# Kernel optimization log

Hardware: AMD Instinct MI355X
Metric: run time of the kernel (lower is better)

Reference implementation:

```python
import jax, jax.numpy as jnp
import numpy as np

H = 160      # hidden_size
NH = 8       # num_heads
HD = H // NH # per_head_size = 20
MAXLEN = 512 # max_seq_len (pe tables have 2*MAXLEN+1 rows)
FF = 640     # ffn inner size
B, S = 4, 256


def setup_inputs():
    key = jax.random.key(0)
    ks = jax.random.split(key, 24)
    def rn(k, shape, scale=0.02):
        return jax.random.normal(k, shape, dtype=jnp.float32) * scale
    tbl = 2 * MAXLEN + 1
    d = dict(
        inp=jax.random.normal(ks[0], (B, S, H), dtype=jnp.float32),
        pos_s=jnp.sort(jax.random.randint(ks[1], (B, S), 0, S), axis=-1),
        pos_e=jnp.sort(jax.random.randint(ks[2], (B, S), 0, S), axis=-1),
        seq_len=jax.random.randint(ks[3], (B,), S // 2, S + 1),
        lex_num=0,
        pe_ss=rn(ks[4], (tbl, H), 1.0), pe_se=rn(ks[5], (tbl, H), 1.0),
        pe_es=rn(ks[6], (tbl, H), 1.0), pe_ee=rn(ks[7], (tbl, H), 1.0),
        W_fus=rn(ks[8], (4 * H, H)), b_fus=jnp.zeros((H,), jnp.float32),
        Wq=rn(ks[9], (H, H)), bq=jnp.zeros((H,), jnp.float32),
        Wk=rn(ks[10], (H, H)), bk=jnp.zeros((H,), jnp.float32),
        Wv=rn(ks[11], (H, H)), bv=jnp.zeros((H,), jnp.float32),
        Wr=rn(ks[12], (H, H)), br=jnp.zeros((H,), jnp.float32),
        u=rn(ks[13], (NH, HD), 0.1), v=rn(ks[14], (NH, HD), 0.1),
        W_fin=rn(ks[15], (H, H)), b_fin=jnp.zeros((H,), jnp.float32),
        ln1_g=jnp.ones((H,), jnp.float32), ln1_b=jnp.zeros((H,), jnp.float32),
        W1=rn(ks[16], (H, FF)), b1=jnp.zeros((FF,), jnp.float32),
        W2=rn(ks[17], (FF, H)), b2=jnp.zeros((H,), jnp.float32),
        ln2_g=jnp.ones((H,), jnp.float32), ln2_b=jnp.zeros((H,), jnp.float32),
    )
    return d


def _ln(x, g, b, eps=1e-5):
    mu = jnp.mean(x, axis=-1, keepdims=True)
    var = jnp.mean((x - mu) ** 2, axis=-1, keepdims=True)
    return (x - mu) * jax.lax.rsqrt(var + eps) * g + b


def reference(inp, pos_s, pos_e, seq_len, lex_num, pe_ss, pe_se, pe_es, pe_ee,
              W_fus, b_fus, Wq, bq, Wk, bk, Wv, bv, Wr, br, u, v,
              W_fin, b_fin, ln1_g, ln1_b, W1, b1, W2, b2, ln2_g, ln2_b):
    Bb, Ss, Hh = inp.shape
    # ---- Four_Pos_Fusion_Embedding, fusion='ff' ----
    dss = pos_s[:, :, None] - pos_s[:, None, :] + MAXLEN  # [B,S,S] indices
    dse = pos_s[:, :, None] - pos_e[:, None, :] + MAXLEN
    des = pos_e[:, :, None] - pos_s[:, None, :] + MAXLEN
    dee = pos_e[:, :, None] - pos_e[:, None, :] + MAXLEN
    pe4 = jnp.concatenate([pe_ss[dss], pe_se[dse], pe_es[des], pe_ee[dee]], axis=-1)  # [B,S,S,4H]
    rel = jax.nn.relu(pe4 @ W_fus + b_fus)  # [B,S,S,H]
    # ---- MultiHead_Attention_Lattice_rel (Transformer-XL style) ----
    q = (inp @ Wq + bq).reshape(Bb, Ss, NH, HD).transpose(0, 2, 1, 3)   # [B,H,S,d]
    k = (inp @ Wk + bk).reshape(Bb, Ss, NH, HD).transpose(0, 2, 1, 3)
    val = (inp @ Wv + bv).reshape(Bb, Ss, NH, HD).transpose(0, 2, 1, 3)
    r = (rel @ Wr + br).reshape(Bb, Ss, Ss, NH, HD)                     # [B,Sq,Sk,H,d]
    A_C = jnp.einsum('bhid,bhjd->bhij', q + u[None, :, None, :], k)
    B_D = jnp.einsum('bhid,bijhd->bhij', q + v[None, :, None, :], r)
    scores = (A_C + B_D) / np.float32(np.sqrt(HD))
    mask = jnp.arange(Ss)[None, :] < (seq_len + lex_num)[:, None]       # [B,S]
    scores = jnp.where(mask[:, None, None, :], scores, jnp.float32(-1e15))
    attn = jax.nn.softmax(scores, axis=-1)
    out = jnp.einsum('bhij,bhjd->bhid', attn, val)
    out = out.transpose(0, 2, 1, 3).reshape(Bb, Ss, Hh)
    out = out @ W_fin + b_fin
    # ---- Layer_Process 'an': output = LN(output + output) (as written in source) ----
    out = _ln(out + out, ln1_g, ln1_b)
    # ---- PositionWise_FeedForward ----
    ff = jax.nn.relu(out @ W1 + b1) @ W2 + b2
    out2 = _ln(ff + ff, ln2_g, ln2_b)
    return out2
```

## Files before the change

### kernel.cpp

```cpp
#include <hip/hip_runtime.h>
#include <hip/hip_bf16.h>
#include <math.h>

#define SS    256
#define BB    4
#define HH    160
#define NH_   8
#define HD_   20
#define TBL   1025
#define MAXL  512
#define FF_   640
#define PROWS 512

#define PT_TILES 64
#define PT_PER_TAB (PT_TILES * 3)
#define PT_END (4 * PT_PER_TAB)
#define QKV_END (PT_END + 512)
#define WRT_END (QKV_END + 100)

__device__ __forceinline__ float blo(unsigned x) {
  return __uint_as_float(x << 16);
}
__device__ __forceinline__ float bhi(unsigned x) {
  return __uint_as_float(x & 0xffff0000u);
}

__global__ __launch_bounds__(256) void k_setup(
    const float* __restrict__ pe_ss, const float* __restrict__ pe_se,
    const float* __restrict__ pe_es, const float* __restrict__ pe_ee,
    const float* __restrict__ W_fus, const float* __restrict__ b_fus,
    const float* __restrict__ inp,
    const float* __restrict__ Wq, const float* __restrict__ bq,
    const float* __restrict__ Wk, const float* __restrict__ bk,
    const float* __restrict__ Wv, const float* __restrict__ bv,
    const float* __restrict__ Wr,
    __hip_bfloat16* __restrict__ Pbf, float* __restrict__ qb,
    float* __restrict__ kb, float* __restrict__ vb, float* __restrict__ WrT) {
  int bid = blockIdx.x;
  int t = threadIdx.x;
  __shared__ __align__(16) float As[16][HH];

  if (bid < PT_END) {
    int tab = bid / PT_PER_TAB;
    int rem = bid - tab * PT_PER_TAB;
    int tile = rem / 3, yc = rem - tile * 3;
    int row0 = 256 + tile * 8;
    const float* pe = (tab == 0) ? pe_ss : (tab == 1) ? pe_se
                    : (tab == 2) ? pe_es : pe_ee;
    for (int idx = t; idx < 8 * 40; idx += 256) {
      int r = idx / 40, c4 = idx - r * 40;
      *(float4*)&As[r][c4 * 4] =
          *(const float4*)(pe + (size_t)(row0 + r) * HH + c4 * 4);
    }
    __syncthreads();
    int c = (t & 63) + yc * 64;
    int wv = t >> 6;
    if (c < HH) {
      float acc0, acc1;
      acc0 = acc1 = (tab == 0) ? b_fus[c] : 0.0f;
      const float* wp = W_fus + (size_t)tab * HH * HH + c;
      int r0 = wv * 2, r1 = wv * 2 + 1;
      #pragma unroll 2
      for (int k = 0; k < HH; k += 8) {
        float w[8];
        #pragma unroll
        for (int q = 0; q < 8; ++q) w[q] = wp[(size_t)(k + q) * HH];
        float4 a0 = *(const float4*)&As[r0][k];
        float4 a1 = *(const float4*)&As[r0][k + 4];
        float4 b0 = *(const float4*)&As[r1][k];
        float4 b1_ = *(const float4*)&As[r1][k + 4];
        acc0 = fmaf(a0.x, w[0], acc0); acc0 = fmaf(a0.y, w[1], acc0);
        acc0 = fmaf(a0.z, w[2], acc0); acc0 = fmaf(a0.w, w[3], acc0);
        acc0 = fmaf(a1.x, w[4], acc0); acc0 = fmaf(a1.y, w[5], acc0);
        acc0 = fmaf(a1.z, w[6], acc0); acc0 = fmaf(a1.w, w[7], acc0);
        acc1 = fmaf(b0.x, w[0], acc1); acc1 = fmaf(b0.y, w[1], acc1);
        acc1 = fmaf(b0.z, w[2], acc1); acc1 = fmaf(b0.w, w[3], acc1);
        acc1 = fmaf(b1_.x, w[4], acc1); acc1 = fmaf(b1_.y, w[5], acc1);
        acc1 = fmaf(b1_.z, w[6], acc1); acc1 = fmaf(b1_.w, w[7], acc1);
      }
      int rloc = tile * 8;
      Pbf[((size_t)tab * PROWS + rloc + r0) * HH + c] = __float2bfloat16(acc0);
      Pbf[((size_t)tab * PROWS + rloc + r1) * HH + c] = __float2bfloat16(acc1);
    }
  } else if (bid < QKV_END) {
    int qbid = bid - PT_END;
    int bx = qbid & 63, by = qbid >> 6;
    int tok0 = bx * 16;
    {
      const float4* src = (const float4*)(inp + (size_t)tok0 * HH);
      float4* dst = (float4*)As;
      for (int idx = t; idx < 16 * HH / 4; idx += 256) dst[idx] = src[idx];
    }
    __syncthreads();
    int col = (t & 63) + by * 64;
    int wv = t >> 6;
    if (col < 480) {
      int mat = col / 160;
      int c = col - mat * 160;
      const float* W   = (mat == 0) ? Wq : (mat == 1) ? Wk : Wv;
      const float* bia = (mat == 0) ? bq : (mat == 1) ? bk : bv;
      float* O         = (mat == 0) ? qb : (mat == 1) ? kb : vb;
      float acc[4];
      float bb = bia[c];
      #pragma unroll
      for (int i = 0; i < 4; ++i) acc[i] = bb;
      const float* wp = W + c;
      #pragma unroll 2
      for (int k = 0; k < HH; k += 8) {
        float w[8];
        #pragma unroll
        for (int q = 0; q < 8; ++q) w[q] = wp[(size_t)(k + q) * HH];
        #pragma unroll
        for (int i = 0; i < 4; ++i) {
          const float4 a0 = *(const float4*)&As[wv * 4 + i][k];
          const float4 a1 = *(const float4*)&As[wv * 4 + i][k + 4];
          acc[i] = fmaf(a0.x, w[0], acc[i]);
          acc[i] = fmaf(a0.y, w[1], acc[i]);
          acc[i] = fmaf(a0.z, w[2], acc[i]);
          acc[i] = fmaf(a0.w, w[3], acc[i]);
          acc[i] = fmaf(a1.x, w[4], acc[i]);
          acc[i] = fmaf(a1.y, w[5], acc[i]);
          acc[i] = fmaf(a1.z, w[6], acc[i]);
          acc[i] = fmaf(a1.w, w[7], acc[i]);
        }
      }
      #pragma unroll
      for (int i = 0; i < 4; ++i)
        O[(size_t)(tok0 + wv * 4 + i) * HH + c] = acc[i];
    }
  } else {
    int o = (bid - QKV_END) * 256 + t;
    int cp = o / HH, cc = o - cp * HH;
    WrT[o] = Wr[(size_t)cc * HH + cp];
  }
}

__global__ __launch_bounds__(256) void k_gmat(
    const float* __restrict__ qb, const float* __restrict__ vtab,
    const float* __restrict__ WrT, __hip_bfloat16* __restrict__ gmat_bf) {
  const int T = 4;
  int tok0 = blockIdx.x * T;
  int t = threadIdx.x;
  __shared__ __align__(16) float qs[T][HH];
  if (t < T * HH / 4) {
    int tt = t / 40, c4 = t - tt * 40;
    float4 q4 = *(const float4*)(qb + (size_t)(tok0 + tt) * HH + c4 * 4);
    float4 v4 = *(const float4*)(vtab + c4 * 4);
    q4.x += v4.x; q4.y += v4.y; q4.z += v4.z; q4.w += v4.w;
    *(float4*)&qs[tt][c4 * 4] = q4;
  }
  __syncthreads();
  #pragma unroll
  for (int r = 0; r < 5; ++r) {
    int p = r * 256 + t;
    int h = p / HH, cc = p - h * HH;
    float acc0 = 0.f, acc1 = 0.f, acc2 = 0.f, acc3 = 0.f;
    const float* wp = WrT + (size_t)(h * HD_) * HH + cc;
    #pragma unroll 4
    for (int d = 0; d < HD_; ++d) {
      float w = wp[(size_t)d * HH];
      acc0 = fmaf(qs[0][h * HD_ + d], w, acc0);
      acc1 = fmaf(qs[1][h * HD_ + d], w, acc1);
      acc2 = fmaf(qs[2][h * HD_ + d], w, acc2);
      acc3 = fmaf(qs[3][h * HD_ + d], w, acc3);
    }
    gmat_bf[(size_t)(tok0 + 0) * (NH_ * HH) + p] = __float2bfloat16(acc0);
    gmat_bf[(size_t)(tok0 + 1) * (NH_ * HH) + p] = __float2bfloat16(acc1);
    gmat_bf[(size_t)(tok0 + 2) * (NH_ * HH) + p] = __float2bfloat16(acc2);
    gmat_bf[(size_t)(tok0 + 3) * (NH_ * HH) + p] = __float2bfloat16(acc3);
  }
}

template<int TT, int KK, bool RELU>
__global__ __launch_bounds__(256) void k_gemm(
    const float* __restrict__ A, const float* __restrict__ W,
    const float* __restrict__ bias, float* __restrict__ C, int N) {
  const int TPW = TT / 4;
  int tok0 = blockIdx.x * TT;
  int t = threadIdx.x;
  __shared__ __align__(16) float As[TT][KK];
  {
    const float4* src = (const float4*)(A + (size_t)tok0 * KK);
    float4* dst = (float4*)As;
    for (int idx = t; idx < TT * KK / 4; idx += 256) dst[idx] = src[idx];
  }
  __syncthreads();
  int c = (t & 63) + blockIdx.y * 64;
  int wv = t >> 6;
  if (c < N) {
    float acc[TPW];
    float bb = bias ? bias[c] : 0.0f;
    #pragma unroll
    for (int i = 0; i < TPW; ++i) acc[i] = bb;
    const float* wp = W + c;
    #pragma unroll 2
    for (int k = 0; k < KK; k += 8) {
      float w[8];
      #pragma unroll
      for (int q = 0; q < 8; ++q) w[q] = wp[(size_t)(k + q) * N];
      #pragma unroll
      for (int i = 0; i < TPW; ++i) {
        const float4 a0 = *(const float4*)&As[wv * TPW + i][k];
        const float4 a1 = *(const float4*)&As[wv * TPW + i][k + 4];
        acc[i] = fmaf(a0.x, w[0], acc[i]);
        acc[i] = fmaf(a0.y, w[1], acc[i]);
        acc[i] = fmaf(a0.z, w[2], acc[i]);
        acc[i] = fmaf(a0.w, w[3], acc[i]);
        acc[i] = fmaf(a1.x, w[4], acc[i]);
        acc[i] = fmaf(a1.y, w[5], acc[i]);
        acc[i] = fmaf(a1.z, w[6], acc[i]);
        acc[i] = fmaf(a1.w, w[7], acc[i]);
      }
    }
    #pragma unroll
    for (int i = 0; i < TPW; ++i) {
      float v = RELU ? fmaxf(acc[i], 0.0f) : acc[i];
      C[(size_t)(tok0 + wv * TPW + i) * N + c] = v;
    }
  }
}

__global__ __launch_bounds__(256) void k_ffn1(
    const float* __restrict__ Y, const float* __restrict__ g1,
    const float* __restrict__ b1ln, const float* __restrict__ W1,
    const float* __restrict__ b1, float* __restrict__ Hb) {
  const int TT = 16;
  int tok0 = blockIdx.x * TT;
  int t = threadIdx.x;
  __shared__ __align__(16) float As[TT][HH];
  {
    const float4* src = (const float4*)(Y + (size_t)tok0 * HH);
    float4* dst = (float4*)As;
    for (int idx = t; idx < TT * HH / 4; idx += 256) dst[idx] = src[idx];
  }
  __syncthreads();
  {
    int row = t >> 4, l = t & 15;
    float s = 0.0f;
    #pragma unroll
    for (int c = l; c < HH; c += 16) s += As[row][c];
    #pragma unroll
    for (int m = 1; m < 16; m <<= 1) s += __shfl_xor(s, m);
    float mu = s * (1.0f / HH);
    float s2 = 0.0f;
    #pragma unroll
    for (int c = l; c < HH; c += 16) { float d = As[row][c] - mu; s2 = fmaf(d, d, s2); }
    #pragma unroll
    for (int m = 1; m < 16; m <<= 1) s2 += __shfl_xor(s2, m);
    float rstd = rsqrtf(s2 * (1.0f / HH) + 2.5e-6f);
    #pragma unroll
    for (int c = l; c < HH; c += 16)
      As[row][c] = (As[row][c] - mu) * rstd * g1[c] + b1ln[c];
  }
  __syncthreads();
  int c = (t & 63) + blockIdx.y * 64;
  int wv = t >> 6;
  float acc[4];
  float bb = b1[c];
  #pragma unroll
  for (int i = 0; i < 4; ++i) acc[i] = bb;
  const float* wp = W1 + c;
  #pragma unroll 2
  for (int k = 0; k < HH; k += 8) {
    float w[8];
    #pragma unroll
    for (int q = 0; q < 8; ++q) w[q] = wp[(size_t)(k + q) * FF_];
    #pragma unroll
    for (int i = 0; i < 4; ++i) {
      const float4 a0 = *(const float4*)&As[wv * 4 + i][k];
      const float4 a1 = *(const float4*)&As[wv * 4 + i][k + 4];
      acc[i] = fmaf(a0.x, w[0], acc[i]);
      acc[i] = fmaf(a0.y, w[1], acc[i]);
      acc[i] = fmaf(a0.z, w[2], acc[i]);
      acc[i] = fmaf(a0.w, w[3], acc[i]);
      acc[i] = fmaf(a1.x, w[4], acc[i]);
      acc[i] = fmaf(a1.y, w[5], acc[i]);
      acc[i] = fmaf(a1.z, w[6], acc[i]);
      acc[i] = fmaf(a1.w, w[7], acc[i]);
    }
  }
  #pragma unroll
  for (int i = 0; i < 4; ++i)
    Hb[(size_t)(tok0 + wv * 4 + i) * FF_ + c] = fmaxf(acc[i], 0.0f);
}

#define RSTR 164
#define SCP  132

__global__ __launch_bounds__(256, 4) void k_score(
    const float* __restrict__ qb, const float* __restrict__ kb,
    const __hip_bfloat16* __restrict__ gmat_bf,
    const __hip_bfloat16* __restrict__ Pbf,
    const int* __restrict__ pos_s, const int* __restrict__ pos_e,
    const int* __restrict__ seq_len, const int* __restrict__ lex_num,
    const float* __restrict__ utab, float* __restrict__ scores) {
  int bid = blockIdx.x;
  int blk = bid >> 1;
  int half = bid & 1;
  int b = blk >> 8;
  int i = blk & 255;
  int t = threadIdx.x;
  int limit = seq_len[b] + lex_num[0];
  if (half * 128 >= limit) return;

  __shared__ __align__(16) float qu[HH];
  __shared__ __align__(16) float g_s[NH_][RSTR];
  __shared__ __align__(16) float sc_s[NH_][SCP];
  __shared__ int ps_s[SS], pe_s[SS];

  if (t < HH) qu[t] = qb[(size_t)blk * HH + t] + utab[t];
  ps_s[t] = pos_s[b * SS + t];
  pe_s[t] = pos_e[b * SS + t];
  if (t < 160) {
    const uint4* gsrc = (const uint4*)(gmat_bf + (size_t)blk * (NH_ * HH));
    uint4 u = gsrc[t];
    int h = t / 20, c8 = (t - h * 20) * 8;
    g_s[h][c8 + 0] = blo(u.x); g_s[h][c8 + 1] = bhi(u.x);
    g_s[h][c8 + 2] = blo(u.y); g_s[h][c8 + 3] = bhi(u.y);
    g_s[h][c8 + 4] = blo(u.z); g_s[h][c8 + 5] = bhi(u.z);
    g_s[h][c8 + 6] = blo(u.w); g_s[h][c8 + 7] = bhi(u.w);
  }
  __syncthreads();

  int w = t >> 6, lane = t & 63;
  int jj = lane >> 2, cg = lane & 3;
  int psi = ps_s[i], pei = pe_s[i];
  const float scale = 0.22360679774997896f;

  const uint4* Pb0 = (const uint4*)Pbf;
  const uint4* Pb1 = Pb0 + (size_t)PROWS * 20;
  const uint4* Pb2 = Pb1 + (size_t)PROWS * 20;
  const uint4* Pb3 = Pb2 + (size_t)PROWS * 20;
  const float4* kb4 = (const float4*)(kb + (size_t)b * SS * HH);

  #pragma unroll
  for (int pass = 0; pass < 2; ++pass) {
    int tau = (pass == 0) ? w : 7 - w;
    int jl = tau * 16 + jj;
    int j = half * 128 + jl;
    if (half * 128 + tau * 16 >= limit) continue;
    int psj = ps_s[j], pej = pe_s[j];
    int r0b = (psi - psj + 256) * 20;
    int r1b = (psi - pej + 256) * 20;
    int r2b = (pei - psj + 256) * 20;
    int r3b = (pei - pej + 256) * 20;
    float bd[NH_];
    #pragma unroll
    for (int h = 0; h < NH_; ++h) bd[h] = 0.0f;
    #pragma unroll 2
    for (int q5 = 0; q5 < 5; ++q5) {
      int off = q5 * 4 + cg;
      uint4 u0 = Pb0[r0b + off];
      uint4 u1 = Pb1[r1b + off];
      uint4 u2 = Pb2[r2b + off];
      uint4 u3 = Pb3[r3b + off];
      float rl[8];
      rl[0] = fmaxf(blo(u0.x) + blo(u1.x) + blo(u2.x) + blo(u3.x), 0.0f);
      rl[1] = fmaxf(bhi(u0.x) + bhi(u1.x) + bhi(u2.x) + bhi(u3.x), 0.0f);
      rl[2] = fmaxf(blo(u0.y) + blo(u1.y) + blo(u2.y) + blo(u3.y), 0.0f);
      rl[3] = fmaxf(bhi(u0.y) + bhi(u1.y) + bhi(u2.y) + bhi(u3.y), 0.0f);
      rl[4] = fmaxf(blo(u0.z) + blo(u1.z) + blo(u2.z) + blo(u3.z), 0.0f);
      rl[5] = fmaxf(bhi(u0.z) + bhi(u1.z) + bhi(u2.z) + bhi(u3.z), 0.0f);
      rl[6] = fmaxf(blo(u0.w) + blo(u1.w) + blo(u2.w) + blo(u3.w), 0.0f);
      rl[7] = fmaxf(bhi(u0.w) + bhi(u1.w) + bhi(u2.w) + bhi(u3.w), 0.0f);
      int cb = off * 8;
      #pragma unroll
      for (int h = 0; h < NH_; ++h) {
        float4 ga = *(const float4*)&g_s[h][cb];
        float4 gb = *(const float4*)&g_s[h][cb + 4];
        bd[h] = fmaf(rl[0], ga.x, bd[h]);
        bd[h] = fmaf(rl[1], ga.y, bd[h]);
        bd[h] = fmaf(rl[2], ga.z, bd[h]);
        bd[h] = fmaf(rl[3], ga.w, bd[h]);
        bd[h] = fmaf(rl[4], gb.x, bd[h]);
        bd[h] = fmaf(rl[5], gb.y, bd[h]);
        bd[h] = fmaf(rl[6], gb.z, bd[h]);
        bd[h] = fmaf(rl[7], gb.w, bd[h]);
      }
    }
    float ac0 = 0.0f, ac1 = 0.0f;
    {
      int kbase = j * 40 + 10 * cg;
      #pragma unroll
      for (int m = 0; m < 10; ++m) {
        float4 kv = kb4[kbase + m];
        float4 q4 = *(const float4*)&qu[(10 * cg + m) * 4];
        if (m < 5) {
          ac0 = fmaf(q4.x, kv.x, ac0); ac0 = fmaf(q4.y, kv.y, ac0);
          ac0 = fmaf(q4.z, kv.z, ac0); ac0 = fmaf(q4.w, kv.w, ac0);
        } else {
          ac1 = fmaf(q4.x, kv.x, ac1); ac1 = fmaf(q4.y, kv.y, ac1);
          ac1 = fmaf(q4.z, kv.z, ac1); ac1 = fmaf(q4.w, kv.w, ac1);
        }
      }
    }
    #pragma unroll
    for (int h = 0; h < NH_; ++h) {
      bd[h] += __shfl_xor(bd[h], 1);
      bd[h] += __shfl_xor(bd[h], 2);
    }
    float s0, s1;
    if      (cg == 0) { s0 = bd[0]; s1 = bd[1]; }
    else if (cg == 1) { s0 = bd[2]; s1 = bd[3]; }
    else if (cg == 2) { s0 = bd[4]; s1 = bd[5]; }
    else              { s0 = bd[6]; s1 = bd[7]; }
    sc_s[2 * cg][jl]     = (s0 + ac0) * scale;
    sc_s[2 * cg + 1][jl] = (s1 + ac1) * scale;
  }
  __syncthreads();

  {
    int row = t >> 5, c4 = t & 31;
    float4 v = *(const float4*)&sc_s[row][c4 * 4];
    *(float4*)&scores[((size_t)blk * NH_ + row) * SS + half * 128 + c4 * 4] = v;
  }
}

#define SCS 260

__global__ __launch_bounds__(256, 4) void k_smpv(
    const float* __restrict__ scores, const float* __restrict__ vb,
    const int* __restrict__ seq_len, const int* __restrict__ lex_num,
    const float* __restrict__ W_fin, const float* __restrict__ b_fin,
    float* __restrict__ ybuf) {
  int blk = blockIdx.x;
  int b = blk >> 8;
  int t = threadIdx.x;
  __shared__ __align__(16) float sc[NH_][SCS];
  __shared__ __align__(16) float outs[HH];
  int limit = seq_len[b] + lex_num[0];

  const float4* src = (const float4*)(scores + (size_t)blk * NH_ * SS);
  #pragma unroll
  for (int r = 0; r < 2; ++r) {
    int idx = r * 256 + t;
    int row = idx >> 6, c4 = idx & 63;
    float4 v = src[idx];
    int j0 = c4 * 4;
    v.x = (j0 + 0 < limit) ? v.x : -1.0e15f;
    v.y = (j0 + 1 < limit) ? v.y : -1.0e15f;
    v.z = (j0 + 2 < limit) ? v.z : -1.0e15f;
    v.w = (j0 + 3 < limit) ? v.w : -1.0e15f;
    *(float4*)&sc[row][j0] = v;
  }
  __syncthreads();

  {
    int h = t >> 5, l = t & 31;
    float m = -3.0e38f;
    float e[8];
    #pragma unroll
    for (int ii = 0; ii < 8; ++ii) m = fmaxf(m, sc[h][l + ii * 32]);
    #pragma unroll
    for (int msk = 16; msk; msk >>= 1) m = fmaxf(m, __shfl_xor(m, msk));
    float s = 0.0f;
    #pragma unroll
    for (int ii = 0; ii < 8; ++ii) { e[ii] = __expf(sc[h][l + ii * 32] - m); s += e[ii]; }
    #pragma unroll
    for (int msk = 16; msk; msk >>= 1) s += __shfl_xor(s, msk);
    float inv = 1.0f / s;
    #pragma unroll
    for (int ii = 0; ii < 8; ++ii) sc[h][l + ii * 32] = e[ii] * inv;
  }
  __syncthreads();

  if (t < HH) {
    int h = t / HD_;
    int lim4 = (limit + 3) & ~3;
    float acc0 = 0.f, acc1 = 0.f, acc2 = 0.f, acc3 = 0.f;
    const float* vcol = vb + (size_t)b * SS * HH + t;
    for (int j2 = 0; j2 < lim4; j2 += 4) {
      float4 p4 = *(const float4*)&sc[h][j2];
      acc0 = fmaf(p4.x, vcol[(size_t)(j2 + 0) * HH], acc0);
      acc1 = fmaf(p4.y, vcol[(size_t)(j2 + 1) * HH], acc1);
      acc2 = fmaf(p4.z, vcol[(size_t)(j2 + 2) * HH], acc2);
      acc3 = fmaf(p4.w, vcol[(size_t)(j2 + 3) * HH], acc3);
    }
    outs[t] = (acc0 + acc1) + (acc2 + acc3);
  }
  __syncthreads();

  if (t < HH) {
    float acc = b_fin[t];
    const float* wp = W_fin + t;
    #pragma unroll 8
    for (int c = 0; c < HH; ++c)
      acc = fmaf(outs[c], wp[(size_t)c * HH], acc);
    ybuf[(size_t)blk * HH + t] = acc;
  }
}

__global__ __launch_bounds__(256) void k_ln(
    const float* __restrict__ Y, const float* __restrict__ g,
    const float* __restrict__ bln, float* __restrict__ O) {
  int tok = blockIdx.x * 4 + (threadIdx.x >> 6);
  int l = threadIdx.x & 63;
  const float* y = Y + (size_t)tok * HH;
  float a = y[l];
  float bv = y[l + 64];
  bool has3 = l < (HH - 128);
  float cv = has3 ? y[l + 128] : 0.0f;
  float s = a + bv + cv;
  #pragma unroll
  for (int m = 32; m; m >>= 1) s += __shfl_xor(s, m);
  float mu = s * (1.0f / HH);
  float da = a - mu, db = bv - mu, dc = has3 ? (cv - mu) : 0.0f;
  float s2 = da * da + db * db + dc * dc;
  #pragma unroll
  for (int m = 32; m; m >>= 1) s2 += __shfl_xor(s2, m);
  float rstd = rsqrtf(s2 * (1.0f / HH) + 2.5e-6f);
  float* o = O + (size_t)tok * HH;
  o[l]      = da * rstd * g[l] + bln[l];
  o[l + 64] = db * rstd * g[l + 64] + bln[l + 64];
  if (has3) o[l + 128] = dc * rstd * g[l + 128] + bln[l + 128];
}

extern "C" void kernel_launch(void* const* d_in, const int* in_sizes, int n_in,
                              void* d_out, int out_size, void* d_ws, size_t ws_size,
                              hipStream_t stream) {
  const float* inp    = (const float*)d_in[0];
  const int*   pos_s  = (const int*)d_in[1];
  const int*   pos_e  = (const int*)d_in[2];
  const int*   seq_ln = (const int*)d_in[3];
  const int*   lex_nm = (const int*)d_in[4];
  const float* pe_ss  = (const float*)d_in[5];
  const float* pe_se  = (const float*)d_in[6];
  const float* pe_es  = (const float*)d_in[7];
  const float* pe_ee  = (const float*)d_in[8];
  const float* W_fus  = (const float*)d_in[9];
  const float* b_fus  = (const float*)d_in[10];
  const float* Wq     = (const float*)d_in[11];
  const float* bq     = (const float*)d_in[12];
  const float* Wk     = (const float*)d_in[13];
  const float* bk     = (const float*)d_in[14];
  const float* Wv     = (const float*)d_in[15];
  const float* bv     = (const float*)d_in[16];
  const float* Wr     = (const float*)d_in[17];
  const float* utab   = (const float*)d_in[19];
  const float* vtab   = (const float*)d_in[20];
  const float* W_fin  = (const float*)d_in[21];
  const float* b_fin  = (const float*)d_in[22];
  const float* ln1_g  = (const float*)d_in[23];
  const float* ln1_b  = (const float*)d_in[24];
  const float* W1     = (const float*)d_in[25];
  const float* b1     = (const float*)d_in[26];
  const float* W2     = (const float*)d_in[27];
  const float* b2     = (const float*)d_in[28];
  const float* ln2_g  = (const float*)d_in[29];
  const float* ln2_b  = (const float*)d_in[30];

  float* ws = (float*)d_ws;
  __hip_bfloat16* Pbf = (__hip_bfloat16*)ws;
  float* qb       = ws + 163840;
  float* kb       = qb + BB * SS * HH;
  float* vb       = kb + BB * SS * HH;
  float* WrT      = vb + BB * SS * HH;
  float* gregion  = WrT + HH * HH;
  __hip_bfloat16* gmat_bf = (__hip_bfloat16*)gregion;
  float* ybuf     = gregion;
  float* scores   = gregion + 655360;
  float* hbuf     = scores;
  float* y2       = scores + 655360;

  (void)in_sizes; (void)n_in; (void)out_size; (void)ws_size;

  const int M = BB * SS;

  k_setup<<<WRT_END, 256, 0, stream>>>(pe_ss, pe_se, pe_es, pe_ee, W_fus, b_fus,
                                       inp, Wq, bq, Wk, bk, Wv, bv, Wr,
                                       Pbf, qb, kb, vb, WrT);
  k_gmat<<<M / 4, 256, 0, stream>>>(qb, vtab, WrT, gmat_bf);
  k_score<<<2 * M, 256, 0, stream>>>(qb, kb, gmat_bf, Pbf, pos_s, pos_e,
                                     seq_ln, lex_nm, utab, scores);
  k_smpv<<<M, 256, 0, stream>>>(scores, vb, seq_ln, lex_nm, W_fin, b_fin, ybuf);
  k_ffn1<<<dim3(M / 16, 10), 256, 0, stream>>>(ybuf, ln1_g, ln1_b, W1, b1, hbuf);
  k_gemm<4, FF_, false><<<dim3(M / 4, 3), 256, 0, stream>>>(hbuf, W2, b2, y2, HH);
  k_ln<<<M / 4, 256, 0, stream>>>(y2, ln2_g, ln2_b, (float*)d_out);
}
```

Baseline: 114.8 us.

## Split score kernel into quarter-row blocks and split-K the W2 GEMM

Result: no change. 115.3 us (+0.4%).

```diff
diff --git a/kernel.cpp b/kernel.cpp
--- a/kernel.cpp
+++ b/kernel.cpp
@@ -171,55 +171,6 @@
   }
 }
 
-template<int TT, int KK, bool RELU>
-__global__ __launch_bounds__(256) void k_gemm(
-    const float* __restrict__ A, const float* __restrict__ W,
-    const float* __restrict__ bias, float* __restrict__ C, int N) {
-  const int TPW = TT / 4;
-  int tok0 = blockIdx.x * TT;
-  int t = threadIdx.x;
-  __shared__ __align__(16) float As[TT][KK];
-  {
-    const float4* src = (const float4*)(A + (size_t)tok0 * KK);
-    float4* dst = (float4*)As;
-    for (int idx = t; idx < TT * KK / 4; idx += 256) dst[idx] = src[idx];
-  }
-  __syncthreads();
-  int c = (t & 63) + blockIdx.y * 64;
-  int wv = t >> 6;
-  if (c < N) {
-    float acc[TPW];
-    float bb = bias ? bias[c] : 0.0f;
-    #pragma unroll
-    for (int i = 0; i < TPW; ++i) acc[i] = bb;
-    const float* wp = W + c;
-    #pragma unroll 2
-    for (int k = 0; k < KK; k += 8) {
-      float w[8];
-      #pragma unroll
-      for (int q = 0; q < 8; ++q) w[q] = wp[(size_t)(k + q) * N];
-      #pragma unroll
-      for (int i = 0; i < TPW; ++i) {
-        const float4 a0 = *(const float4*)&As[wv * TPW + i][k];
-        const float4 a1 = *(const float4*)&As[wv * TPW + i][k + 4];
-        acc[i] = fmaf(a0.x, w[0], acc[i]);
-        acc[i] = fmaf(a0.y, w[1], acc[i]);
-        acc[i] = fmaf(a0.z, w[2], acc[i]);
-        acc[i] = fmaf(a0.w, w[3], acc[i]);
-        acc[i] = fmaf(a1.x, w[4], acc[i]);
-        acc[i] = fmaf(a1.y, w[5], acc[i]);
-        acc[i] = fmaf(a1.z, w[6], acc[i]);
-        acc[i] = fmaf(a1.w, w[7], acc[i]);
-      }
-    }
-    #pragma unroll
-    for (int i = 0; i < TPW; ++i) {
-      float v = RELU ? fmaxf(acc[i], 0.0f) : acc[i];
-      C[(size_t)(tok0 + wv * TPW + i) * N + c] = v;
-    }
-  }
-}
-
 __global__ __launch_bounds__(256) void k_ffn1(
     const float* __restrict__ Y, const float* __restrict__ g1,
     const float* __restrict__ b1ln, const float* __restrict__ W1,
@@ -284,8 +235,51 @@
     Hb[(size_t)(tok0 + wv * 4 + i) * FF_ + c] = fmaxf(acc[i], 0.0f);
 }
 
+__global__ __launch_bounds__(256) void k_w2(
+    const float* __restrict__ A, const float* __restrict__ W2,
+    const float* __restrict__ b2, float* __restrict__ y2a,
+    float* __restrict__ y2b) {
+  const int TT = 4, KH = 320;
+  int tok0 = blockIdx.x * TT;
+  int kz = blockIdx.z;
+  int t = threadIdx.x;
+  __shared__ __align__(16) float As[TT][KH];
+  {
+    const float* src = A + (size_t)tok0 * FF_ + kz * KH;
+    for (int idx = t; idx < TT * KH / 4; idx += 256) {
+      int tt = idx / (KH / 4), c4 = idx - tt * (KH / 4);
+      *(float4*)&As[tt][c4 * 4] = *(const float4*)(src + (size_t)tt * FF_ + c4 * 4);
+    }
+  }
+  __syncthreads();
+  int c = (t & 63) + blockIdx.y * 64;
+  int wv = t >> 6;
+  if (c < HH) {
+    float acc = (kz == 0) ? b2[c] : 0.0f;
+    const float* wp = W2 + (size_t)(kz * KH) * HH + c;
+    #pragma unroll 2
+    for (int k = 0; k < KH; k += 8) {
+      float w[8];
+      #pragma unroll
+      for (int q = 0; q < 8; ++q) w[q] = wp[(size_t)(k + q) * HH];
+      const float4 a0 = *(const float4*)&As[wv][k];
+      const float4 a1 = *(const float4*)&As[wv][k + 4];
+      acc = fmaf(a0.x, w[0], acc);
+      acc = fmaf(a0.y, w[1], acc);
+      acc = fmaf(a0.z, w[2], acc);
+      acc = fmaf(a0.w, w[3], acc);
+      acc = fmaf(a1.x, w[4], acc);
+      acc = fmaf(a1.y, w[5], acc);
+      acc = fmaf(a1.z, w[6], acc);
+      acc = fmaf(a1.w, w[7], acc);
+    }
+    float* O = (kz == 0) ? y2a : y2b;
+    O[(size_t)(tok0 + wv) * HH + c] = acc;
+  }
+}
+
 #define RSTR 164
-#define SCP  132
+#define SCP  68
 
 __global__ __launch_bounds__(256, 4) void k_score(
     const float* __restrict__ qb, const float* __restrict__ kb,
@@ -295,13 +289,13 @@
     const int* __restrict__ seq_len, const int* __restrict__ lex_num,
     const float* __restrict__ utab, float* __restrict__ scores) {
   int bid = blockIdx.x;
-  int blk = bid >> 1;
-  int half = bid & 1;
+  int blk = bid >> 2;
+  int qtr = bid & 3;
   int b = blk >> 8;
   int i = blk & 255;
   int t = threadIdx.x;
   int limit = seq_len[b] + lex_num[0];
-  if (half * 128 >= limit) return;
+  if (qtr * 64 >= limit) return;
 
   __shared__ __align__(16) float qu[HH];
   __shared__ __align__(16) float g_s[NH_][RSTR];
@@ -333,12 +327,9 @@
   const uint4* Pb3 = Pb2 + (size_t)PROWS * 20;
   const float4* kb4 = (const float4*)(kb + (size_t)b * SS * HH);
 
-  #pragma unroll
-  for (int pass = 0; pass < 2; ++pass) {
-    int tau = (pass == 0) ? w : 7 - w;
-    int jl = tau * 16 + jj;
-    int j = half * 128 + jl;
-    if (half * 128 + tau * 16 >= limit) continue;
+  int jl = w * 16 + jj;
+  int j = qtr * 64 + jl;
+  if (qtr * 64 + w * 16 < limit) {
     int psj = ps_s[j], pej = pe_s[j];
     int r0b = (psi - psj + 256) * 20;
     int r1b = (psi - pej + 256) * 20;
@@ -409,10 +400,10 @@
   }
   __syncthreads();
 
-  {
-    int row = t >> 5, c4 = t & 31;
+  if (t < 128) {
+    int row = t >> 4, c4 = t & 15;
     float4 v = *(const float4*)&sc_s[row][c4 * 4];
-    *(float4*)&scores[((size_t)blk * NH_ + row) * SS + half * 128 + c4 * 4] = v;
+    *(float4*)&scores[((size_t)blk * NH_ + row) * SS + qtr * 64 + c4 * 4] = v;
   }
 }
 
@@ -490,16 +481,18 @@
   }
 }
 
-__global__ __launch_bounds__(256) void k_ln(
-    const float* __restrict__ Y, const float* __restrict__ g,
-    const float* __restrict__ bln, float* __restrict__ O) {
+__global__ __launch_bounds__(256) void k_ln2(
+    const float* __restrict__ Ya, const float* __restrict__ Yb,
+    const float* __restrict__ g, const float* __restrict__ bln,
+    float* __restrict__ O) {
   int tok = blockIdx.x * 4 + (threadIdx.x >> 6);
   int l = threadIdx.x & 63;
-  const float* y = Y + (size_t)tok * HH;
-  float a = y[l];
-  float bv = y[l + 64];
+  const float* ya = Ya + (size_t)tok * HH;
+  const float* yb = Yb + (size_t)tok * HH;
+  float a = ya[l] + yb[l];
+  float bv = ya[l + 64] + yb[l + 64];
   bool has3 = l < (HH - 128);
-  float cv = has3 ? y[l + 128] : 0.0f;
+  float cv = has3 ? (ya[l + 128] + yb[l + 128]) : 0.0f;
   float s = a + bv + cv;
   #pragma unroll
   for (int m = 32; m; m >>= 1) s += __shfl_xor(s, m);
@@ -560,7 +553,8 @@
   float* ybuf     = gregion;
   float* scores   = gregion + 655360;
   float* hbuf     = scores;
-  float* y2       = scores + 655360;
+  float* y2a      = scores + 655360;
+  float* y2b      = scores + 819200;
 
   (void)in_sizes; (void)n_in; (void)out_size; (void)ws_size;
 
@@ -570,10 +564,10 @@
                                        inp, Wq, bq, Wk, bk, Wv, bv, Wr,
                                        Pbf, qb, kb, vb, WrT);
   k_gmat<<<M / 4, 256, 0, stream>>>(qb, vtab, WrT, gmat_bf);
-  k_score<<<2 * M, 256, 0, stream>>>(qb, kb, gmat_bf, Pbf, pos_s, pos_e,
+  k_score<<<4 * M, 256, 0, stream>>>(qb, kb, gmat_bf, Pbf, pos_s, pos_e,
                                      seq_ln, lex_nm, utab, scores);
   k_smpv<<<M, 256, 0, stream>>>(scores, vb, seq_ln, lex_nm, W_fin, b_fin, ybuf);
   k_ffn1<<<dim3(M / 16, 10), 256, 0, stream>>>(ybuf, ln1_g, ln1_b, W1, b1, hbuf);
-  k_gemm<4, FF_, false><<<dim3(M / 4, 3), 256, 0, stream>>>(hbuf, W2, b2, y2, HH);
-  k_ln<<<M / 4, 256, 0, stream>>>(y2, ln2_g, ln2_b, (float*)d_out);
-}
+  k_w2<<<dim3(M / 4, 3, 2), 256, 0, stream>>>(hbuf, W2, b2, y2a, y2b);
+  k_ln2<<<M / 4, 256, 0, stream>>>(y2a, y2b, ln2_g, ln2_b, (float*)d_out);
+}
```
